# Optimization experiments

Hardware: AMD Instinct MI355X
Metric: run time of the kernel (lower is better)

Reference implementation:

```python
import jax, jax.numpy as jnp
import numpy as np

B, I, N = 512, 128, 256
ODE_UNFOLDS = 6

def setup_inputs() -> dict:
    key = jax.random.key(0)
    ks = jax.random.split(key, 16)
    u = lambda k, shape, lo, hi: jax.random.uniform(k, shape, jnp.float32, lo, hi)
    inputs = jax.random.normal(ks[0], (B, I), jnp.float32)
    state = jax.random.normal(ks[1], (B, N), jnp.float32)
    sensory_mu = u(ks[2], (I, N), 0.3, 0.8)
    sensory_sigma = u(ks[3], (I, N), 3.0, 8.0)
    sensory_W = u(ks[4], (I, N), 0.01, 1.0)
    sensory_erev = (2.0 * jax.random.randint(ks[5], (I, N), 0, 2).astype(jnp.float32) - 1.0)
    mu = u(ks[6], (N, N), 0.3, 0.8)
    sigma = u(ks[7], (N, N), 3.0, 8.0)
    W = u(ks[8], (N, N), 0.01, 1.0)
    erev = (2.0 * jax.random.randint(ks[9], (N, N), 0, 2).astype(jnp.float32) - 1.0)
    vleak = u(ks[10], (N,), -0.2, 0.2)
    gleak = jnp.ones((N,), jnp.float32)         # gleak_init_min == gleak_init_max == 1.0
    cm_t = jnp.full((N,), 0.5, jnp.float32)     # cm_init_min == cm_init_max == 0.5
    return dict(inputs=inputs, state=state, sensory_mu=sensory_mu,
                sensory_sigma=sensory_sigma, sensory_W=sensory_W,
                sensory_erev=sensory_erev, mu=mu, sigma=sigma, W=W, erev=erev,
                vleak=vleak, gleak=gleak, cm_t=cm_t)

def reference(inputs, state, sensory_mu, sensory_sigma, sensory_W, sensory_erev,
              mu, sigma, W, erev, vleak, gleak, cm_t):
    # sensory gating: (B, I, N)
    s_act = sensory_W * jax.nn.sigmoid(sensory_sigma * (inputs[:, :, None] - sensory_mu))
    w_num_sensory = jnp.sum(s_act * sensory_erev, axis=1)  # (B, N)
    w_den_sensory = jnp.sum(s_act, axis=1)                 # (B, N)

    def step(v_pre, _):
        # recurrent gating: (B, N, N)
        w_act = W * jax.nn.sigmoid(sigma * (v_pre[:, :, None] - mu))
        w_num = jnp.sum(w_act * erev, axis=1) + w_num_sensory
        w_den = jnp.sum(w_act, axis=1) + w_den_sensory
        numerator = cm_t * v_pre + gleak * vleak + w_num
        denominator = cm_t + gleak + w_den
        return numerator / denominator, None

    v, _ = jax.lax.scan(step, state, None, length=ODE_UNFOLDS)
    return (v, v)
```

## Files before the change

kernel.cpp:

```cpp
#include <hip/hip_runtime.h>
#include <stdint.h>

#define NN 256
#define II 128
#define BATCH 512
#define STEPS 6
#define LOG2E 1.4426950408889634f

typedef float v2f __attribute__((ext_vector_type(2)));

__device__ __forceinline__ unsigned short f2bf(float x) {
    unsigned u = __builtin_bit_cast(unsigned, x);
    u += 0x7FFFu + ((u >> 16) & 1u);
    return (unsigned short)(u >> 16);
}
__device__ __forceinline__ float bflo(unsigned u) { return __builtin_bit_cast(float, u << 16); }
__device__ __forceinline__ float bfhi(unsigned u) { return __builtin_bit_cast(float, u & 0xFFFF0000u); }

__global__ void pack4(const float* __restrict__ sigma, const float* __restrict__ mu,
                      const float* __restrict__ W, const float* __restrict__ erev,
                      uint4* __restrict__ out, int rows)
{
    int idx = blockIdx.x * blockDim.x + threadIdx.x;
    if (idx >= (rows / 2) * NN) return;
    int ip = idx >> 8, j = idx & (NN - 1);
    int k0 = (ip * 2) * NN + j, k1 = k0 + NN;
    float sg0 = sigma[k0], sg1 = sigma[k1];
    float p0 = -LOG2E * sg0, q0 = LOG2E * sg0 * mu[k0];
    float p1 = -LOG2E * sg1, q1 = LOG2E * sg1 * mu[k1];
    float w0 = W[k0] * erev[k0], w1 = W[k1] * erev[k1];
    uint4 u;
    u.x = ((unsigned)f2bf(q0) << 16) | (unsigned)f2bf(p0);
    u.y = ((unsigned)f2bf(q1) << 16) | (unsigned)f2bf(p1);
    u.z = ((unsigned)f2bf(w1) << 16) | (unsigned)f2bf(w0);
    u.w = ((unsigned)f2bf(fabsf(w1)) << 16) | (unsigned)f2bf(fabsf(w0));
    out[idx] = u;
}

__global__ __launch_bounds__(1024, 4)
void ltc_packed(const float* __restrict__ inputs, const float* __restrict__ state,
                const uint4* __restrict__ sw4, const uint4* __restrict__ rw4,
                const float* __restrict__ vleak, const float* __restrict__ gleak,
                const float* __restrict__ cm, float* __restrict__ out)
{
    __shared__ __align__(16) float v_sh[2][NN];
    __shared__ __align__(16) float x_sh[2][II];
    __shared__ float2 sens_sh[2][NN];
    __shared__ float2 part[8][NN];

    const int tid  = threadIdx.x;
    const int j    = tid & (NN - 1);
    const int q    = tid >> 8;
    const int row0 = blockIdx.x * 2;

    if (tid < 2 * NN) {
        int r = tid >> 8, c = tid & (NN - 1);
        v_sh[r][c] = state[(row0 + r) * NN + c];
    } else if (tid < 2 * NN + 2 * II) {
        int t = tid - 2 * NN;
        x_sh[t >> 7][t & (II - 1)] = inputs[(row0 + (t >> 7)) * II + (t & (II - 1))];
    }

    const int r2 = tid >> 8;
    float cmv = 0.f, glvl = 0.f, denb = 0.f;
    if (tid < 512) {
        float c = cm[j], g = gleak[j];
        cmv = c; glvl = g * vleak[j]; denb = c + g;
    }
    __syncthreads();

    {
        v2f sn[2] = {{0.f,0.f},{0.f,0.f}}, sd[2] = {{0.f,0.f},{0.f,0.f}};
        #pragma unroll 4
        for (int ip = 0; ip < 16; ++ip) {
            const int i = (q * 16 + ip) * 2;
            uint4 u = sw4[(q * 16 + ip) * NN + j];
            v2f p01 = {bflo(u.x), bflo(u.y)};
            v2f q01 = {bfhi(u.x), bfhi(u.y)};
            v2f ws  = {bflo(u.z), bfhi(u.z)};
            v2f wa  = {bflo(u.w), bfhi(u.w)};
            #pragma unroll
            for (int r = 0; r < 2; ++r) {
                v2f x01 = *(const v2f*)(&x_sh[r][i]);
                v2f arg = __builtin_elementwise_fma(p01, x01, q01);
                v2f e; e.x = __builtin_amdgcn_exp2f(arg.x); e.y = __builtin_amdgcn_exp2f(arg.y);
                v2f b = e + 1.0f;
                float rr = __builtin_amdgcn_rcpf(b.x * b.y);
                v2f bs = __builtin_shufflevector(b, b, 1, 0);
                v2f rs = {rr, rr};
                v2f ms = ws * bs;
                v2f ma = wa * bs;
                sn[r] = __builtin_elementwise_fma(ms, rs, sn[r]);
                sd[r] = __builtin_elementwise_fma(ma, rs, sd[r]);
            }
        }
        part[q * 2 + 0][j] = make_float2(sn[0].x + sn[0].y, sd[0].x + sd[0].y);
        part[q * 2 + 1][j] = make_float2(sn[1].x + sn[1].y, sd[1].x + sd[1].y);
    }
    __syncthreads();
    if (tid < 512) {
        float2 a0 = part[0 + r2][j], a1 = part[2 + r2][j], a2 = part[4 + r2][j], a3 = part[6 + r2][j];
        sens_sh[r2][j] = make_float2(a0.x + a1.x + a2.x + a3.x, a0.y + a1.y + a2.y + a3.y);
    }
    __syncthreads();

    for (int step = 0; step < STEPS; ++step) {
        v2f sn[2] = {{0.f,0.f},{0.f,0.f}}, sd[2] = {{0.f,0.f},{0.f,0.f}};
        #pragma unroll 4
        for (int ip = 0; ip < 32; ++ip) {
            const int i = (q * 32 + ip) * 2;
            uint4 u = rw4[(q * 32 + ip) * NN + j];
            v2f p01 = {bflo(u.x), bflo(u.y)};
            v2f q01 = {bfhi(u.x), bfhi(u.y)};
            v2f ws  = {bflo(u.z), bfhi(u.z)};
            v2f wa  = {bflo(u.w), bfhi(u.w)};
            #pragma unroll
            for (int r = 0; r < 2; ++r) {
                v2f v01 = *(const v2f*)(&v_sh[r][i]);
                v2f arg = __builtin_elementwise_fma(p01, v01, q01);
                v2f e; e.x = __builtin_amdgcn_exp2f(arg.x); e.y = __builtin_amdgcn_exp2f(arg.y);
                v2f b = e + 1.0f;
                float rr = __builtin_amdgcn_rcpf(b.x * b.y);
                v2f bs = __builtin_shufflevector(b, b, 1, 0);
                v2f rs = {rr, rr};
                v2f ms = ws * bs;
                v2f ma = wa * bs;
                sn[r] = __builtin_elementwise_fma(ms, rs, sn[r]);
                sd[r] = __builtin_elementwise_fma(ma, rs, sd[r]);
            }
        }
        part[q * 2 + 0][j] = make_float2(sn[0].x + sn[0].y, sd[0].x + sd[0].y);
        part[q * 2 + 1][j] = make_float2(sn[1].x + sn[1].y, sd[1].x + sd[1].y);
        __syncthreads();

        if (tid < 512) {
            float2 a0 = part[0 + r2][j], a1 = part[2 + r2][j], a2 = part[4 + r2][j], a3 = part[6 + r2][j];
            float wn = a0.x + a1.x + a2.x + a3.x + sens_sh[r2][j].x;
            float wd = a0.y + a1.y + a2.y + a3.y + sens_sh[r2][j].y;
            float vp = v_sh[r2][j];
            float vn = (fmaf(cmv, vp, glvl) + wn) * __builtin_amdgcn_rcpf(denb + wd);
            v_sh[r2][j] = vn;
            if (step == STEPS - 1) {
                out[(row0 + r2) * NN + j] = vn;
                out[BATCH * NN + (row0 + r2) * NN + j] = vn;
            }
        }
        __syncthreads();
    }
}

__global__ __launch_bounds__(1024, 4)
void ltc_fallback(const float* __restrict__ inputs, const float* __restrict__ state,
                  const float* __restrict__ s_sigma, const float* __restrict__ s_mu,
                  const float* __restrict__ s_W, const float* __restrict__ s_erev,
                  const float* __restrict__ r_sigma, const float* __restrict__ r_mu,
                  const float* __restrict__ r_W, const float* __restrict__ r_erev,
                  const float* __restrict__ vleak, const float* __restrict__ gleak,
                  const float* __restrict__ cm, float* __restrict__ out)
{
    __shared__ float  v_sh[2][NN];
    __shared__ float  x_sh[2][II];
    __shared__ float2 sens_sh[2][NN];
    __shared__ float2 part[8][NN];

    const int tid  = threadIdx.x;
    const int j    = tid & (NN - 1);
    const int q    = tid >> 8;
    const int row0 = blockIdx.x * 2;

    if (tid < 2 * NN) {
        int r = tid >> 8, c = tid & (NN - 1);
        v_sh[r][c] = state[(row0 + r) * NN + c];
    } else if (tid < 2 * NN + 2 * II) {
        int t = tid - 2 * NN;
        x_sh[t >> 7][t & (II - 1)] = inputs[(row0 + (t >> 7)) * II + (t & (II - 1))];
    }

    const int r2 = tid >> 8;
    float cmv = 0.f, glvl = 0.f, denb = 0.f;
    if (tid < 512) {
        float c = cm[j], g = gleak[j];
        cmv = c; glvl = g * vleak[j]; denb = c + g;
    }
    __syncthreads();

    {
        float sn[2] = {0.f, 0.f}, sd[2] = {0.f, 0.f};
        for (int ii = 0; ii < 32; ++ii) {
            const int i = q * 32 + ii;
            int k = i * NN + j;
            float sg = s_sigma[k];
            float p = -LOG2E * sg, qq = LOG2E * sg * s_mu[k];
            float w = s_W[k] * s_erev[k];
            #pragma unroll
            for (int r = 0; r < 2; ++r) {
                float e = __builtin_amdgcn_exp2f(fmaf(p, x_sh[r][i], qq));
                float t = w * __builtin_amdgcn_rcpf(1.f + e);
                sn[r] += t; sd[r] += fabsf(t);
            }
        }
        part[q * 2 + 0][j] = make_float2(sn[0], sd[0]);
        part[q * 2 + 1][j] = make_float2(sn[1], sd[1]);
    }
    __syncthreads();
    if (tid < 512) {
        float2 a0 = part[0 + r2][j], a1 = part[2 + r2][j], a2 = part[4 + r2][j], a3 = part[6 + r2][j];
        sens_sh[r2][j] = make_float2(a0.x + a1.x + a2.x + a3.x, a0.y + a1.y + a2.y + a3.y);
    }
    __syncthreads();

    for (int step = 0; step < STEPS; ++step) {
        float sn[2] = {0.f, 0.f}, sd[2] = {0.f, 0.f};
        for (int ii = 0; ii < 64; ++ii) {
            const int i = q * 64 + ii;
            int k = i * NN + j;
            float sg = r_sigma[k];
            float p = -LOG2E * sg, qq = LOG2E * sg * r_mu[k];
            float w = r_W[k] * r_erev[k];
            #pragma unroll
            for (int r = 0; r < 2; ++r) {
                float e = __builtin_amdgcn_exp2f(fmaf(p, v_sh[r][i], qq));
                float t = w * __builtin_amdgcn_rcpf(1.f + e);
                sn[r] += t; sd[r] += fabsf(t);
            }
        }
        part[q * 2 + 0][j] = make_float2(sn[0], sd[0]);
        part[q * 2 + 1][j] = make_float2(sn[1], sd[1]);
        __syncthreads();

        if (tid < 512) {
            float2 a0 = part[0 + r2][j], a1 = part[2 + r2][j], a2 = part[4 + r2][j], a3 = part[6 + r2][j];
            float wn = a0.x + a1.x + a2.x + a3.x + sens_sh[r2][j].x;
            float wd = a0.y + a1.y + a2.y + a3.y + sens_sh[r2][j].y;
            float vp = v_sh[r2][j];
            float vn = (fmaf(cmv, vp, glvl) + wn) * __builtin_amdgcn_rcpf(denb + wd);
            v_sh[r2][j] = vn;
            if (step == STEPS - 1) {
                out[(row0 + r2) * NN + j] = vn;
                out[BATCH * NN + (row0 + r2) * NN + j] = vn;
            }
        }
        __syncthreads();
    }
}

extern "C" void kernel_launch(void* const* d_in, const int* in_sizes, int n_in,
                              void* d_out, int out_size, void* d_ws, size_t ws_size,
                              hipStream_t stream)
{
    const float* inputs  = (const float*)d_in[0];
    const float* state   = (const float*)d_in[1];
    const float* s_mu    = (const float*)d_in[2];
    const float* s_sigma = (const float*)d_in[3];
    const float* s_W     = (const float*)d_in[4];
    const float* s_erev  = (const float*)d_in[5];
    const float* mu      = (const float*)d_in[6];
    const float* sigma   = (const float*)d_in[7];
    const float* W       = (const float*)d_in[8];
    const float* erev    = (const float*)d_in[9];
    const float* vleak   = (const float*)d_in[10];
    const float* gleak   = (const float*)d_in[11];
    const float* cm      = (const float*)d_in[12];
    float* out = (float*)d_out;

    const size_t need = ((NN / 2) * NN + (II / 2) * NN) * sizeof(uint4);
    if (ws_size >= need) {
        uint4* rw4 = (uint4*)d_ws;
        uint4* sw4 = rw4 + (NN / 2) * NN;
        pack4<<<(NN / 2), 256, 0, stream>>>(sigma, mu, W, erev, rw4, NN);
        pack4<<<(II / 2), 256, 0, stream>>>(s_sigma, s_mu, s_W, s_erev, sw4, II);
        ltc_packed<<<BATCH / 2, 1024, 0, stream>>>(inputs, state, sw4, rw4,
                                                   vleak, gleak, cm, out);
    } else {
        ltc_fallback<<<BATCH / 2, 1024, 0, stream>>>(
            inputs, state, s_sigma, s_mu, s_W, s_erev, sigma, mu, W, erev,
            vleak, gleak, cm, out);
    }
}
```

Baseline: 86.13 us.

## Repack weights as fp16 with thread-interleaved layout, one row per block

Parameters are now packed as fp16 (p,q pairs plus signed W·erev, with |w| computed on the fly) in a layout where four adjacent threads split the reduction over i for one output neuron. Partial sums are combined with wave shuffles instead of a shared-memory partial buffer. Each block now handles one batch row instead of two, v is double-buffered so each step needs a single barrier, and launch bounds ask for higher occupancy. Per-row weight traffic rises because the two-row reuse is gone, which the smaller fp16 footprint and the lighter reduction are meant to offset. fp16 may also lose precision on the sigmoid arguments.

Result: faster. 78.07 us (-9.4%).

```diff
diff --git a/kernel.cpp b/kernel.cpp
--- a/kernel.cpp
+++ b/kernel.cpp
@@ -7,145 +7,125 @@
 #define STEPS 6
 #define LOG2E 1.4426950408889634f
 
+typedef _Float16 half_t;
+typedef _Float16 h2 __attribute__((ext_vector_type(2)));
 typedef float v2f __attribute__((ext_vector_type(2)));
 
-__device__ __forceinline__ unsigned short f2bf(float x) {
-    unsigned u = __builtin_bit_cast(unsigned, x);
-    u += 0x7FFFu + ((u >> 16) & 1u);
-    return (unsigned short)(u >> 16);
-}
-__device__ __forceinline__ float bflo(unsigned u) { return __builtin_bit_cast(float, u << 16); }
-__device__ __forceinline__ float bfhi(unsigned u) { return __builtin_bit_cast(float, u & 0xFFFF0000u); }
-
-__global__ void pack4(const float* __restrict__ sigma, const float* __restrict__ mu,
-                      const float* __restrict__ W, const float* __restrict__ erev,
-                      uint4* __restrict__ out, int rows)
-{
-    int idx = blockIdx.x * blockDim.x + threadIdx.x;
-    if (idx >= (rows / 2) * NN) return;
-    int ip = idx >> 8, j = idx & (NN - 1);
-    int k0 = (ip * 2) * NN + j, k1 = k0 + NN;
-    float sg0 = sigma[k0], sg1 = sigma[k1];
-    float p0 = -LOG2E * sg0, q0 = LOG2E * sg0 * mu[k0];
-    float p1 = -LOG2E * sg1, q1 = LOG2E * sg1 * mu[k1];
-    float w0 = W[k0] * erev[k0], w1 = W[k1] * erev[k1];
-    uint4 u;
-    u.x = ((unsigned)f2bf(q0) << 16) | (unsigned)f2bf(p0);
-    u.y = ((unsigned)f2bf(q1) << 16) | (unsigned)f2bf(p1);
-    u.z = ((unsigned)f2bf(w1) << 16) | (unsigned)f2bf(w0);
-    u.w = ((unsigned)f2bf(fabsf(w1)) << 16) | (unsigned)f2bf(fabsf(w0));
-    out[idx] = u;
-}
-
-__global__ __launch_bounds__(1024, 4)
-void ltc_packed(const float* __restrict__ inputs, const float* __restrict__ state,
-                const uint4* __restrict__ sw4, const uint4* __restrict__ rw4,
-                const float* __restrict__ vleak, const float* __restrict__ gleak,
-                const float* __restrict__ cm, float* __restrict__ out)
+__global__ void pack_f16(const float* __restrict__ sigma, const float* __restrict__ mu,
+                         const float* __restrict__ W, const float* __restrict__ erev,
+                         uint4* __restrict__ pq4, uint2* __restrict__ w2, int ni)
+{
+    int gid = blockIdx.x * blockDim.x + threadIdx.x;
+    int total = (ni / 16) * 1024;
+    if (gid >= total) return;
+    int ip2 = gid >> 10, t = gid & 1023;
+    int q = t & 3, j = t >> 2;
+    int i0 = q * (ni / 4) + ip2 * 4;
+    unsigned pw[4];
+    half_t wa[4];
+    #pragma unroll
+    for (int e = 0; e < 4; ++e) {
+        int k = (i0 + e) * NN + j;
+        float sg = sigma[k];
+        h2 pq = { (half_t)(-LOG2E * sg), (half_t)(LOG2E * sg * mu[k]) };
+        pw[e] = __builtin_bit_cast(unsigned, pq);
+        wa[e] = (half_t)(W[k] * erev[k]);
+    }
+    pq4[gid] = make_uint4(pw[0], pw[1], pw[2], pw[3]);
+    h2 w01 = { wa[0], wa[1] }, w23 = { wa[2], wa[3] };
+    w2[gid] = make_uint2(__builtin_bit_cast(unsigned, w01),
+                         __builtin_bit_cast(unsigned, w23));
+}
+
+__device__ __forceinline__ void proc_pair(unsigned pq0, unsigned pq1, unsigned wp,
+                                          float va, float vb, v2f& an, v2f& ad)
+{
+    h2 P0 = __builtin_bit_cast(h2, pq0);
+    h2 P1 = __builtin_bit_cast(h2, pq1);
+    h2 Wh = __builtin_bit_cast(h2, wp);
+    float e0 = __builtin_amdgcn_exp2f(fmaf((float)P0.x, va, (float)P0.y));
+    float e1 = __builtin_amdgcn_exp2f(fmaf((float)P1.x, vb, (float)P1.y));
+    float b0 = e0 + 1.f, b1 = e1 + 1.f;
+    float rr = __builtin_amdgcn_rcpf(b0 * b1);
+    float u0 = b1 * rr, u1 = b0 * rr;
+    float w0 = (float)Wh.x, w1 = (float)Wh.y;
+    an.x = fmaf(w0, u0, an.x);
+    an.y = fmaf(w1, u1, an.y);
+    ad.x = fmaf(fabsf(w0), u0, ad.x);
+    ad.y = fmaf(fabsf(w1), u1, ad.y);
+}
+
+__global__ __launch_bounds__(1024, 8)
+void ltc_f16(const float* __restrict__ inputs, const float* __restrict__ state,
+             const uint4* __restrict__ spq, const uint2* __restrict__ sw,
+             const uint4* __restrict__ rpq, const uint2* __restrict__ rw,
+             const float* __restrict__ vleak, const float* __restrict__ gleak,
+             const float* __restrict__ cm, float* __restrict__ out)
 {
     __shared__ __align__(16) float v_sh[2][NN];
-    __shared__ __align__(16) float x_sh[2][II];
-    __shared__ float2 sens_sh[2][NN];
-    __shared__ float2 part[8][NN];
-
-    const int tid  = threadIdx.x;
-    const int j    = tid & (NN - 1);
-    const int q    = tid >> 8;
-    const int row0 = blockIdx.x * 2;
-
-    if (tid < 2 * NN) {
-        int r = tid >> 8, c = tid & (NN - 1);
-        v_sh[r][c] = state[(row0 + r) * NN + c];
-    } else if (tid < 2 * NN + 2 * II) {
-        int t = tid - 2 * NN;
-        x_sh[t >> 7][t & (II - 1)] = inputs[(row0 + (t >> 7)) * II + (t & (II - 1))];
-    }
-
-    const int r2 = tid >> 8;
-    float cmv = 0.f, glvl = 0.f, denb = 0.f;
-    if (tid < 512) {
-        float c = cm[j], g = gleak[j];
-        cmv = c; glvl = g * vleak[j]; denb = c + g;
-    }
-    __syncthreads();
-
+    __shared__ __align__(16) float x_sh[II];
+
+    const int tid = threadIdx.x;
+    const int q   = tid & 3;
+    const int j   = tid >> 2;
+    const int row = blockIdx.x;
+
+    if (tid < II) {
+        x_sh[tid] = inputs[row * II + tid];
+    } else if (tid >= 512 && tid < 512 + NN) {
+        v_sh[0][tid - 512] = state[row * NN + (tid - 512)];
+    }
+    const float c   = cm[j];
+    const float g   = gleak[j];
+    const float glvl = g * vleak[j];
+    const float denb = c + g;
+    __syncthreads();
+
+    float sn, sd;
     {
-        v2f sn[2] = {{0.f,0.f},{0.f,0.f}}, sd[2] = {{0.f,0.f},{0.f,0.f}};
+        v2f an = {0.f, 0.f}, ad = {0.f, 0.f};
+        #pragma unroll
+        for (int ip2 = 0; ip2 < 8; ++ip2) {
+            uint4 u = spq[ip2 * 1024 + tid];
+            uint2 w = sw[ip2 * 1024 + tid];
+            float4 xv = *(const float4*)&x_sh[q * 32 + ip2 * 4];
+            proc_pair(u.x, u.y, w.x, xv.x, xv.y, an, ad);
+            proc_pair(u.z, u.w, w.y, xv.z, xv.w, an, ad);
+        }
+        sn = an.x + an.y;
+        sd = ad.x + ad.y;
+        sn += __shfl_xor(sn, 1, 64); sn += __shfl_xor(sn, 2, 64);
+        sd += __shfl_xor(sd, 1, 64); sd += __shfl_xor(sd, 2, 64);
+    }
+
+    int cur = 0;
+    for (int step = 0; step < STEPS; ++step) {
+        v2f an = {0.f, 0.f}, ad = {0.f, 0.f};
         #pragma unroll 4
-        for (int ip = 0; ip < 16; ++ip) {
-            const int i = (q * 16 + ip) * 2;
-            uint4 u = sw4[(q * 16 + ip) * NN + j];
-            v2f p01 = {bflo(u.x), bflo(u.y)};
-            v2f q01 = {bfhi(u.x), bfhi(u.y)};
-            v2f ws  = {bflo(u.z), bfhi(u.z)};
-            v2f wa  = {bflo(u.w), bfhi(u.w)};
-            #pragma unroll
-            for (int r = 0; r < 2; ++r) {
-                v2f x01 = *(const v2f*)(&x_sh[r][i]);
-                v2f arg = __builtin_elementwise_fma(p01, x01, q01);
-                v2f e; e.x = __builtin_amdgcn_exp2f(arg.x); e.y = __builtin_amdgcn_exp2f(arg.y);
-                v2f b = e + 1.0f;
-                float rr = __builtin_amdgcn_rcpf(b.x * b.y);
-                v2f bs = __builtin_shufflevector(b, b, 1, 0);
-                v2f rs = {rr, rr};
-                v2f ms = ws * bs;
-                v2f ma = wa * bs;
-                sn[r] = __builtin_elementwise_fma(ms, rs, sn[r]);
-                sd[r] = __builtin_elementwise_fma(ma, rs, sd[r]);
-            }
-        }
-        part[q * 2 + 0][j] = make_float2(sn[0].x + sn[0].y, sd[0].x + sd[0].y);
-        part[q * 2 + 1][j] = make_float2(sn[1].x + sn[1].y, sd[1].x + sd[1].y);
-    }
-    __syncthreads();
-    if (tid < 512) {
-        float2 a0 = part[0 + r2][j], a1 = part[2 + r2][j], a2 = part[4 + r2][j], a3 = part[6 + r2][j];
-        sens_sh[r2][j] = make_float2(a0.x + a1.x + a2.x + a3.x, a0.y + a1.y + a2.y + a3.y);
-    }
-    __syncthreads();
-
-    for (int step = 0; step < STEPS; ++step) {
-        v2f sn[2] = {{0.f,0.f},{0.f,0.f}}, sd[2] = {{0.f,0.f},{0.f,0.f}};
-        #pragma unroll 4
-        for (int ip = 0; ip < 32; ++ip) {
-            const int i = (q * 32 + ip) * 2;
-            uint4 u = rw4[(q * 32 + ip) * NN + j];
-            v2f p01 = {bflo(u.x), bflo(u.y)};
-            v2f q01 = {bfhi(u.x), bfhi(u.y)};
-            v2f ws  = {bflo(u.z), bfhi(u.z)};
-            v2f wa  = {bflo(u.w), bfhi(u.w)};
-            #pragma unroll
-            for (int r = 0; r < 2; ++r) {
-                v2f v01 = *(const v2f*)(&v_sh[r][i]);
-                v2f arg = __builtin_elementwise_fma(p01, v01, q01);
-                v2f e; e.x = __builtin_amdgcn_exp2f(arg.x); e.y = __builtin_amdgcn_exp2f(arg.y);
-                v2f b = e + 1.0f;
-                float rr = __builtin_amdgcn_rcpf(b.x * b.y);
-                v2f bs = __builtin_shufflevector(b, b, 1, 0);
-                v2f rs = {rr, rr};
-                v2f ms = ws * bs;
-                v2f ma = wa * bs;
-                sn[r] = __builtin_elementwise_fma(ms, rs, sn[r]);
-                sd[r] = __builtin_elementwise_fma(ma, rs, sd[r]);
-            }
-        }
-        part[q * 2 + 0][j] = make_float2(sn[0].x + sn[0].y, sd[0].x + sd[0].y);
-        part[q * 2 + 1][j] = make_float2(sn[1].x + sn[1].y, sd[1].x + sd[1].y);
+        for (int ip2 = 0; ip2 < 16; ++ip2) {
+            uint4 u = rpq[ip2 * 1024 + tid];
+            uint2 w = rw[ip2 * 1024 + tid];
+            float4 vv = *(const float4*)&v_sh[cur][q * 64 + ip2 * 4];
+            proc_pair(u.x, u.y, w.x, vv.x, vv.y, an, ad);
+            proc_pair(u.z, u.w, w.y, vv.z, vv.w, an, ad);
+        }
+        float rn = an.x + an.y;
+        float rd = ad.x + ad.y;
+        rn += __shfl_xor(rn, 1, 64); rn += __shfl_xor(rn, 2, 64);
+        rd += __shfl_xor(rd, 1, 64); rd += __shfl_xor(rd, 2, 64);
+
+        float wn = rn + sn, wd = rd + sd;
+        float vp = v_sh[cur][j];
+        float vn = (fmaf(c, vp, glvl) + wn) * __builtin_amdgcn_rcpf(denb + wd);
+        if (q == 0) {
+            v_sh[cur ^ 1][j] = vn;
+            if (step == STEPS - 1) {
+                out[row * NN + j] = vn;
+                out[BATCH * NN + row * NN + j] = vn;
+            }
+        }
         __syncthreads();
-
-        if (tid < 512) {
-            float2 a0 = part[0 + r2][j], a1 = part[2 + r2][j], a2 = part[4 + r2][j], a3 = part[6 + r2][j];
-            float wn = a0.x + a1.x + a2.x + a3.x + sens_sh[r2][j].x;
-            float wd = a0.y + a1.y + a2.y + a3.y + sens_sh[r2][j].y;
-            float vp = v_sh[r2][j];
-            float vn = (fmaf(cmv, vp, glvl) + wn) * __builtin_amdgcn_rcpf(denb + wd);
-            v_sh[r2][j] = vn;
-            if (step == STEPS - 1) {
-                out[(row0 + r2) * NN + j] = vn;
-                out[BATCH * NN + (row0 + r2) * NN + j] = vn;
-            }
-        }
-        __syncthreads();
+        cur ^= 1;
     }
 }
 
@@ -169,8 +149,8 @@
     const int row0 = blockIdx.x * 2;
 
     if (tid < 2 * NN) {
-        int r = tid >> 8, c = tid & (NN - 1);
-        v_sh[r][c] = state[(row0 + r) * NN + c];
+        int r = tid >> 8, cc = tid & (NN - 1);
+        v_sh[r][cc] = state[(row0 + r) * NN + cc];
     } else if (tid < 2 * NN + 2 * II) {
         int t = tid - 2 * NN;
         x_sh[t >> 7][t & (II - 1)] = inputs[(row0 + (t >> 7)) * II + (t & (II - 1))];
@@ -179,8 +159,8 @@
     const int r2 = tid >> 8;
     float cmv = 0.f, glvl = 0.f, denb = 0.f;
     if (tid < 512) {
-        float c = cm[j], g = gleak[j];
-        cmv = c; glvl = g * vleak[j]; denb = c + g;
+        float cc = cm[j], gg = gleak[j];
+        cmv = cc; glvl = gg * vleak[j]; denb = cc + gg;
     }
     __syncthreads();
 
@@ -263,14 +243,17 @@
     const float* cm      = (const float*)d_in[12];
     float* out = (float*)d_out;
 
-    const size_t need = ((NN / 2) * NN + (II / 2) * NN) * sizeof(uint4);
+    const size_t need = 16384 * 16 + 16384 * 8 + 8192 * 16 + 8192 * 8;
     if (ws_size >= need) {
-        uint4* rw4 = (uint4*)d_ws;
-        uint4* sw4 = rw4 + (NN / 2) * NN;
-        pack4<<<(NN / 2), 256, 0, stream>>>(sigma, mu, W, erev, rw4, NN);
-        pack4<<<(II / 2), 256, 0, stream>>>(s_sigma, s_mu, s_W, s_erev, sw4, II);
-        ltc_packed<<<BATCH / 2, 1024, 0, stream>>>(inputs, state, sw4, rw4,
-                                                   vleak, gleak, cm, out);
+        char* p = (char*)d_ws;
+        uint4* rpq = (uint4*)p;
+        uint2* rw  = (uint2*)(p + 16384 * 16);
+        uint4* spq = (uint4*)(p + 16384 * 16 + 16384 * 8);
+        uint2* sw  = (uint2*)(p + 16384 * 16 + 16384 * 8 + 8192 * 16);
+        pack_f16<<<64, 256, 0, stream>>>(sigma, mu, W, erev, rpq, rw, NN);
+        pack_f16<<<32, 256, 0, stream>>>(s_sigma, s_mu, s_W, s_erev, spq, sw, II);
+        ltc_f16<<<BATCH, 1024, 0, stream>>>(inputs, state, spq, sw, rpq, rw,
+                                            vleak, gleak, cm, out);
     } else {
         ltc_fallback<<<BATCH / 2, 1024, 0, stream>>>(
             inputs, state, s_sigma, s_mu, s_W, s_erev, sigma, mu, W, erev,
```
